# Optimization experiments

Hardware: AMD Instinct MI355X
Metric: run time of the kernel (lower is better)

## Reference

```python
import jax, jax.numpy as jnp
import numpy as np

B, T, EMB = 2, 2048, 1024
H, D = 16, 64          # n_heads, head_dim; H*D == EMB
FF = 4 * EMB


def _ln(x, w, b, eps=1e-5):
    mu = jnp.mean(x, axis=-1, keepdims=True)
    var = jnp.var(x, axis=-1, keepdims=True)
    return (x - mu) * jax.lax.rsqrt(var + eps) * w + b


def setup_inputs() -> dict:
    key = jax.random.key(0)
    ks = jax.random.split(key, 5)
    s = 0.02
    return {
        "x": jax.random.normal(ks[0], (B, T, EMB), jnp.float32),
        "ln1_w": jnp.ones((EMB,), jnp.float32),
        "ln1_b": jnp.zeros((EMB,), jnp.float32),
        "c_proj_w": jax.random.normal(ks[1], (3 * H * D, EMB), jnp.float32) * s,  # Linear(emb, 3HD, bias=False)
        "proj_w": jax.random.normal(ks[2], (EMB, H * D), jnp.float32) * s,
        "proj_b": jnp.zeros((EMB,), jnp.float32),
        "ln2_w": jnp.ones((EMB,), jnp.float32),
        "ln2_b": jnp.zeros((EMB,), jnp.float32),
        "ffn1_w": jax.random.normal(ks[3], (FF, EMB), jnp.float32) * s,
        "ffn1_b": jnp.zeros((FF,), jnp.float32),
        "ffn2_w": jax.random.normal(ks[4], (EMB, FF), jnp.float32) * s,
        "ffn2_b": jnp.zeros((EMB,), jnp.float32),
    }


def reference(x, ln1_w, ln1_b, c_proj_w, proj_w, proj_b, ln2_w, ln2_b,
              ffn1_w, ffn1_b, ffn2_w, ffn2_b):
    Bx, Tx, C = x.shape
    ln_x = _ln(x, ln1_w, ln1_b)
    c = ln_x @ c_proj_w.T                     # (B,T,3HD)
    c = c.reshape(Bx, Tx, H, 3 * D)
    k, q, v = jnp.split(c, 3, axis=-1)        # split order k,q,v as in source
    q = q.transpose(0, 2, 1, 3)               # (B,H,T,D)
    k = k.transpose(0, 2, 1, 3)
    v = v.transpose(0, 2, 1, 3)
    wei = jnp.einsum('bhqd,bhkd->bhqk', q, k) * (D ** -0.5)  # (B,H,T,T)
    mask = jnp.tril(jnp.ones((Tx, Tx), bool))
    wei = jnp.where(mask, wei, -jnp.inf)
    wei = jax.nn.softmax(wei, axis=-1)
    act = jnp.einsum('bhqk,bhkd->bhqd', wei, v)
    act = act.transpose(0, 2, 1, 3).reshape(Bx, Tx, H * D)
    act = act @ proj_w.T + proj_b
    act = x + act                              # residual 1
    h = _ln(act, ln2_w, ln2_b)
    h = jax.nn.relu(h @ ffn1_w.T + ffn1_b) @ ffn2_w.T + ffn2_b
    return x + h                               # NOTE: source adds x, not act
```

## Files before the change

kernel.cpp:

```cpp
#include <hip/hip_runtime.h>
#include <math.h>

typedef unsigned short u16;
typedef unsigned int u32;
typedef __attribute__((ext_vector_type(8))) __bf16 bf16x8;
typedef __attribute__((ext_vector_type(4))) float f32x4;
typedef __attribute__((ext_vector_type(16))) float f32x16;

#define DEVI __device__ __forceinline__

DEVI u16 f2bf(float f){
  u32 b = __builtin_bit_cast(u32, f);
  return (u16)((b + 0x7FFFu + ((b >> 16) & 1u)) >> 16);
}

DEVI u32 cvtpk(float a, float b){
  u32 r;
  asm("v_cvt_pk_bf16_f32 %0, %1, %2" : "=v"(r) : "v"(a), "v"(b));
  return r;
}

DEVI f32x4 mfma16(bf16x8 a, bf16x8 b, f32x4 c){
  return __builtin_amdgcn_mfma_f32_16x16x32_bf16(a, b, c, 0, 0, 0);
}
DEVI f32x16 mfma32(bf16x8 a, bf16x8 b, f32x16 c){
  return __builtin_amdgcn_mfma_f32_32x32x16_bf16(a, b, c, 0, 0, 0);
}

DEVI void gload16(const u16* g, u16* l){
  __builtin_amdgcn_global_load_lds(
      (const __attribute__((address_space(1))) u32*)g,
      (__attribute__((address_space(3))) u32*)l,
      16, 0, 0);
}

DEVI void phase_bar(){
  __builtin_amdgcn_sched_barrier(0);
  __builtin_amdgcn_s_barrier();
  __builtin_amdgcn_sched_barrier(0);
}

DEVI bf16x8 scale_bf16x8(bf16x8 v, float s){
  u32 w[4]; __builtin_memcpy(w, &v, 16);
  u32 o[4];
  #pragma unroll
  for (int i = 0; i < 4; ++i){
    float f0 = __builtin_bit_cast(float, (w[i] & 0xFFFFu) << 16) * s;
    float f1 = __builtin_bit_cast(float, w[i] & 0xFFFF0000u) * s;
    o[i] = (u32)f2bf(f0) | ((u32)f2bf(f1) << 16);
  }
  bf16x8 r; __builtin_memcpy(&r, o, 16);
  return r;
}

DEVI void cvt_body(const float* __restrict__ in, u16* __restrict__ out, int i){
  float4 v = reinterpret_cast<const float4*>(in)[i];
  u32 lo = (u32)f2bf(v.x) | ((u32)f2bf(v.y) << 16);
  u32 hi = (u32)f2bf(v.z) | ((u32)f2bf(v.w) << 16);
  reinterpret_cast<uint2*>(out)[i] = make_uint2(lo, hi);
}

DEVI void ln_body(const float* __restrict__ x, const float* __restrict__ w,
                  const float* __restrict__ b, u16* __restrict__ out,
                  int row, int tid, float* red){
  const float4 v = reinterpret_cast<const float4*>(x + (size_t)row * 1024)[tid];
  float s  = v.x + v.y + v.z + v.w;
  float ss = v.x*v.x + v.y*v.y + v.z*v.z + v.w*v.w;
  #pragma unroll
  for (int m = 1; m < 64; m <<= 1){
    s  += __shfl_xor(s,  m, 64);
    ss += __shfl_xor(ss, m, 64);
  }
  int wid = tid >> 6, lane = tid & 63;
  if (lane == 0){ red[wid] = s; red[4 + wid] = ss; }
  __syncthreads();
  s  = red[0] + red[1] + red[2] + red[3];
  ss = red[4] + red[5] + red[6] + red[7];
  float mu   = s * (1.0f/1024.0f);
  float var  = ss * (1.0f/1024.0f) - mu*mu;
  float rstd = rsqrtf(var + 1e-5f);
  const float4 wv = reinterpret_cast<const float4*>(w)[tid];
  const float4 bv = reinterpret_cast<const float4*>(b)[tid];
  u32 lo = (u32)f2bf((v.x-mu)*rstd*wv.x + bv.x) | ((u32)f2bf((v.y-mu)*rstd*wv.y + bv.y) << 16);
  u32 hi = (u32)f2bf((v.z-mu)*rstd*wv.z + bv.z) | ((u32)f2bf((v.w-mu)*rstd*wv.w + bv.w) << 16);
  reinterpret_cast<uint2*>(out + (size_t)row*1024)[tid] = make_uint2(lo, hi);
}

__global__ __launch_bounds__(256) void prep_kernel(const float* __restrict__ c_proj_w,
                                                   const float* __restrict__ proj_w,
                                                   const float* __restrict__ ffn1_w,
                                                   const float* __restrict__ ffn2_w,
                                                   const float* __restrict__ x,
                                                   const float* __restrict__ ln1_w,
                                                   const float* __restrict__ ln1_b,
                                                   u16* __restrict__ Wqkv,
                                                   u16* __restrict__ Wproj,
                                                   u16* __restrict__ Wff1,
                                                   u16* __restrict__ Wff2,
                                                   u16* __restrict__ LNb){
  __shared__ float red[8];
  const int bid = blockIdx.x;
  const int tid = threadIdx.x;
  if (bid < 3072){
    cvt_body(c_proj_w, Wqkv, bid*256 + tid);
  } else if (bid < 4096){
    cvt_body(proj_w, Wproj, (bid - 3072)*256 + tid);
  } else if (bid < 8192){
    cvt_body(ffn1_w, Wff1, (bid - 4096)*256 + tid);
  } else if (bid < 12288){
    cvt_body(ffn2_w, Wff2, (bid - 8192)*256 + tid);
  } else {
    ln_body(x, ln1_w, ln1_b, LNb, bid - 12288, tid, red);
  }
}

__global__ __launch_bounds__(256) void ln_kernel(const float* __restrict__ x,
                                                 const float* __restrict__ w,
                                                 const float* __restrict__ b,
                                                 u16* __restrict__ out){
  __shared__ float red[8];
  ln_body(x, w, b, out, blockIdx.x, threadIdx.x, red);
}

__global__ __launch_bounds__(256) void reduce4_kernel(const u16* __restrict__ P,
                                                      const float* __restrict__ x,
                                                      const float* __restrict__ bias,
                                                      float* __restrict__ out){
  const size_t i8 = ((size_t)blockIdx.x * 256 + threadIdx.x) * 8;
  const size_t PS = (size_t)4096 * 1024;
  const int col0 = (int)(i8 & 1023);
  float acc[8];
  #pragma unroll
  for (int j = 0; j < 8; ++j) acc[j] = bias[col0 + j];
  #pragma unroll
  for (int s = 0; s < 4; ++s){
    uint4 d = *reinterpret_cast<const uint4*>(P + s*PS + i8);
    u32 w[4] = {d.x, d.y, d.z, d.w};
    #pragma unroll
    for (int j = 0; j < 8; ++j){
      u32 bits = ((w[j>>1] >> (16*(j&1))) & 0xFFFFu) << 16;
      acc[j] += __builtin_bit_cast(float, bits);
    }
  }
  float4 xv0 = reinterpret_cast<const float4*>(x + i8)[0];
  float4 xv1 = reinterpret_cast<const float4*>(x + i8)[1];
  acc[0]+=xv0.x; acc[1]+=xv0.y; acc[2]+=xv0.z; acc[3]+=xv0.w;
  acc[4]+=xv1.x; acc[5]+=xv1.y; acc[6]+=xv1.z; acc[7]+=xv1.w;
  reinterpret_cast<float4*>(out + i8)[0] = make_float4(acc[0],acc[1],acc[2],acc[3]);
  reinterpret_cast<float4*>(out + i8)[1] = make_float4(acc[4],acc[5],acc[6],acc[7]);
}

template<bool HAS_BIAS, bool RELU, bool SPLIT>
__global__ __launch_bounds__(512, 2) void gemm256(const u16* __restrict__ A,
                                                  const u16* __restrict__ W,
                                                  const float* __restrict__ bias,
                                                  u16* __restrict__ outp,
                                                  int M, int N, int lda, int kLen){
  const int tid = threadIdx.x;
  const int wid = tid >> 6, lane = tid & 63;
  const int l16 = lane & 15, lhi = lane >> 4;
  const int wr = wid >> 2, wc = wid & 3;

  const int gx = gridDim.x, gy = gridDim.y;
  const int nwg = gx * gy * gridDim.z;
  const int bid = (blockIdx.z * gy + blockIdx.y) * gx + blockIdx.x;
  const int swz = (bid & 7) * (nwg >> 3) + (bid >> 3);
  const int col = swz % gx;
  const int rs  = swz / gx;
  const int row = rs % gy;
  const int ksp = rs / gy;
  const int brow = row * 256;
  const int bcol = col * 256;
  const size_t koff = (size_t)ksp * kLen;
  if (SPLIT) outp += (size_t)ksp * M * N;

  __shared__ u16 LDS[2][2][2][256*32];

  const int srow = tid >> 2;
  const int cg   = (tid & 3) ^ ((tid >> 3) & 3);
  const u16* gA = A + (size_t)(brow + srow) * lda + koff + cg*8;
  const u16* gW = W + (size_t)(bcol + srow) * lda + koff + cg*8;
  const size_t rK = (size_t)128 * lda;

#define STAGE(buf, mat, ks, t) do {                                   \
    const u16* _s = ((mat) ? gW : gA) + (t)*64 + (ks)*32;             \
    u16* _d = &LDS[buf][mat][ks][(wid*16)*32];                        \
    gload16(_s,      _d);                                             \
    gload16(_s + rK, _d + 128*32);                                    \
  } while(0)

  const int cswz = (lhi ^ ((l16 >> 1) & 3)) * 8;
  const int aoff = (wr*128 + l16)*32 + cswz;
  const int boff = (wc*64  + l16)*32 + cswz;
#define RDA(buf, ks, m) (*reinterpret_cast<const bf16x8*>(&LDS[buf][0][ks][aoff + (m)*512]))
#define RDB(buf, ks, n) (*reinterpret_cast<const bf16x8*>(&LDS[buf][1][ks][boff + (n)*512]))

  f32x4 acc[8][4] = {};
  bf16x8 a[8], b0, b1;

#define MFMA_PH(n0, n1) do {                                          \
    __builtin_amdgcn_s_setprio(1);                                    \
    _Pragma("unroll")                                                 \
    for (int m = 0; m < 8; ++m){                                      \
      acc[m][n0] = mfma16(a[m], b0, acc[m][n0]);                      \
      acc[m][n1] = mfma16(a[m], b1, acc[m][n1]);                      \
    }                                                                 \
    __builtin_amdgcn_s_setprio(0);                                    \
  } while(0)

  const int NITER = kLen >> 7;

  STAGE(0,0,0,0); STAGE(0,1,0,0); STAGE(0,0,1,0); STAGE(0,1,1,0);
  STAGE(1,0,0,1); STAGE(1,1,0,1);
  asm volatile("s_waitcnt vmcnt(4)" ::: "memory");
  phase_bar();

  for (int j = 0; j < NITER; ++j){
    const int t0 = 2*j, t1 = 2*j + 1;
    const bool more = (j + 1 < NITER);

    #pragma unroll
    for (int m = 0; m < 8; ++m) a[m] = RDA(0,0,m);
    b0 = RDB(0,0,0); b1 = RDB(0,0,1);
    STAGE(1,0,1,t1);
    phase_bar();
    MFMA_PH(0,1);
    phase_bar();
    b0 = RDB(0,0,2); b1 = RDB(0,0,3);
    STAGE(1,1,1,t1);
    phase_bar();
    MFMA_PH(2,3);
    phase_bar();
    #pragma unroll
    for (int m = 0; m < 8; ++m) a[m] = RDA(0,1,m);
    b0 = RDB(0,1,0); b1 = RDB(0,1,1);
    if (more) STAGE(0,0,0,t0+2);
    phase_bar();
    MFMA_PH(0,1);
    phase_bar();
    b0 = RDB(0,1,2); b1 = RDB(0,1,3);
    if (more){ STAGE(0,1,0,t0+2); asm volatile("s_waitcnt vmcnt(4)" ::: "memory"); }
    else     {                    asm volatile("s_waitcnt vmcnt(0)" ::: "memory"); }
    phase_bar();
    MFMA_PH(2,3);
    phase_bar();
    #pragma unroll
    for (int m = 0; m < 8; ++m) a[m] = RDA(1,0,m);
    b0 = RDB(1,0,0); b1 = RDB(1,0,1);
    if (more) STAGE(0,0,1,t0+2);
    phase_bar();
    MFMA_PH(0,1);
    phase_bar();
    b0 = RDB(1,0,2); b1 = RDB(1,0,3);
    if (more) STAGE(0,1,1,t0+2);
    phase_bar();
    MFMA_PH(2,3);
    phase_bar();
    #pragma unroll
    for (int m = 0; m < 8; ++m) a[m] = RDA(1,1,m);
    b0 = RDB(1,1,0); b1 = RDB(1,1,1);
    if (more) STAGE(1,0,0,t1+2);
    phase_bar();
    MFMA_PH(0,1);
    phase_bar();
    b0 = RDB(1,1,2); b1 = RDB(1,1,3);
    if (more){ STAGE(1,1,0,t1+2); asm volatile("s_waitcnt vmcnt(4)" ::: "memory"); }
    phase_bar();
    MFMA_PH(2,3);
    phase_bar();
  }
  __builtin_amdgcn_sched_barrier(0);

  const int row0 = brow + wr*128;
  const int col0 = bcol + wc*64;
  #pragma unroll
  for (int m = 0; m < 8; ++m){
    #pragma unroll
    for (int n = 0; n < 4; ++n){
      #pragma unroll
      for (int r = 0; r < 4; ++r){
        int row_ = row0 + m*16 + 4*lhi + r;
        int col_ = col0 + n*16 + l16;
        float v = acc[m][n][r];
        if constexpr (HAS_BIAS) v += bias[col_];
        if constexpr (RELU)     v = fmaxf(v, 0.0f);
        outp[(size_t)row_ * N + col_] = f2bf(v);
      }
    }
  }
#undef STAGE
#undef RDA
#undef RDB
#undef MFMA_PH
}

template<bool HAS_BIAS, bool HAS_RES, bool RELU, bool OUT_BF16>
__global__ __launch_bounds__(256) void gemm_bt(const u16* __restrict__ A,
                                               const u16* __restrict__ W,
                                               const float* __restrict__ bias,
                                               const float* __restrict__ res,
                                               void* __restrict__ outp,
                                               int M, int N, int K){
  const int tid = threadIdx.x;
  const int wid = tid >> 6, lane = tid & 63;
  const int l16 = lane & 15, lhi = lane >> 4;
  const int wr = wid >> 1, wc = wid & 1;

  const int gx = gridDim.x;
  const int nwg = gx * gridDim.y;
  const int bid = blockIdx.y * gx + blockIdx.x;
  const int swz = (bid & 7) * (nwg >> 3) + (bid >> 3);
  const int brow = (swz / gx) * 128;
  const int bcol = (swz % gx) * 128;

  __shared__ u16 As[2][128*32];
  __shared__ u16 Bs[2][128*32];

  const int srow = wid*32 + (lane >> 2);
  const int schk = lane & 3;
  const u16* gA0 = A + (size_t)(brow + srow)      * K + schk*8;
  const u16* gA1 = A + (size_t)(brow + srow + 16) * K + schk*8;
  const u16* gW0 = W + (size_t)(bcol + srow)      * K + schk*8;
  const u16* gW1 = W + (size_t)(bcol + srow + 16) * K + schk*8;
  const int ldsA0 = (wid*32)*32, ldsA1 = (wid*32 + 16)*32;

  f32x4 acc[4][4] = {};

  gload16(gA0, &As[0][ldsA0]);
  gload16(gA1, &As[0][ldsA1]);
  gload16(gW0, &Bs[0][ldsA0]);
  gload16(gW1, &Bs[0][ldsA1]);

  int cur = 0;
  for (int k0 = 0; k0 < K; k0 += 32){
    __syncthreads();
    if (k0 + 32 < K){
      gload16(gA0 + k0 + 32, &As[cur^1][ldsA0]);
      gload16(gA1 + k0 + 32, &As[cur^1][ldsA1]);
      gload16(gW0 + k0 + 32, &Bs[cur^1][ldsA0]);
      gload16(gW1 + k0 + 32, &Bs[cur^1][ldsA1]);
    }
    bf16x8 af[4], bfr[4];
    #pragma unroll
    for (int m = 0; m < 4; ++m)
      af[m]  = *reinterpret_cast<const bf16x8*>(&As[cur][(wr*64 + m*16 + l16)*32 + 8*lhi]);
    #pragma unroll
    for (int n = 0; n < 4; ++n)
      bfr[n] = *reinterpret_cast<const bf16x8*>(&Bs[cur][(wc*64 + n*16 + l16)*32 + 8*lhi]);
    #pragma unroll
    for (int m = 0; m < 4; ++m){
      #pragma unroll
      for (int n = 0; n < 4; ++n){
        acc[m][n] = mfma16(af[m], bfr[n], acc[m][n]);
      }
    }
    cur ^= 1;
  }

  const int row0 = brow + wr*64;
  const int col0 = bcol + wc*64;
  #pragma unroll
  for (int m = 0; m < 4; ++m){
    #pragma unroll
    for (int n = 0; n < 4; ++n){
      #pragma unroll
      for (int r = 0; r < 4; ++r){
        int row = row0 + m*16 + 4*lhi + r;
        int col = col0 + n*16 + l16;
        float v = acc[m][n][r];
        if constexpr (HAS_BIAS) v += bias[col];
        if constexpr (RELU)     v = fmaxf(v, 0.0f);
        if constexpr (HAS_RES)  v += res[(size_t)row * N + col];
        if constexpr (OUT_BF16) ((u16*)outp)[(size_t)row * N + col] = f2bf(v);
        else                    ((float*)outp)[(size_t)row * N + col] = v;
      }
    }
  }
}

__global__ __launch_bounds__(128) void attn_kernel(const u16* __restrict__ qkv,
                                                   u16* __restrict__ att){
  const int bh = blockIdx.x;
  const int g  = 31 - blockIdx.y;
  const int bb = bh >> 4, hh = bh & 15;
  const int tid = threadIdx.x;
  const int wid = tid >> 6, lane = tid & 63;
  const int l31 = lane & 31, h = lane >> 5;
  const u16* base = qkv + (size_t)bb * 2048 * 3072 + (size_t)hh * 192;

  __shared__ u16 Ks[64*72];
  __shared__ u16 Vt[64*80];

  const int sr = tid >> 1, sh2 = (tid & 1) * 32;
  const u16* kstage = base + (size_t)sr * 3072 + sh2;
  const int va = tid >> 2, vd = (tid & 3) * 16;
  const u16* vstage = base + (size_t)(2*va) * 3072 + 128 + vd;

  const int qrow0 = g*64 + wid*32;
  const int q = qrow0 + l31;

  const float QSCALE = 0.125f * 1.44269504f;
  bf16x8 qb[4];
  {
    const u16* qp = base + (size_t)q * 3072 + 64 + 8*h;
    #pragma unroll
    for (int s = 0; s < 4; ++s)
      qb[s] = scale_bf16x8(*reinterpret_cast<const bf16x8*>(qp + 16*s), QSCALE);
  }

  f32x16 o0 = (f32x16)0.0f, o1 = (f32x16)0.0f;
  float m = -INFINITY, l = 0.0f;

  const int nkt = g + 1;

  uint4 ka0, ka1, ka2, ka3, v00, v01, v10, v11;
  ka0 = *reinterpret_cast<const uint4*>(kstage);
  ka1 = *reinterpret_cast<const uint4*>(kstage + 8);
  ka2 = *reinterpret_cast<const uint4*>(kstage + 16);
  ka3 = *reinterpret_cast<const uint4*>(kstage + 24);
  v00 = *reinterpret_cast<const uint4*>(vstage);
  v01 = *reinterpret_cast<const uint4*>(vstage + 8);
  v10 = *reinterpret_cast<const uint4*>(vstage + 3072);
  v11 = *reinterpret_cast<const uint4*>(vstage + 3072 + 8);

  for (int kt = 0; kt < nkt; ++kt){
    __syncthreads();
    *reinterpret_cast<uint4*>(&Ks[sr*72 + sh2])      = ka0;
    *reinterpret_cast<uint4*>(&Ks[sr*72 + sh2 + 8])  = ka1;
    *reinterpret_cast<uint4*>(&Ks[sr*72 + sh2 + 16]) = ka2;
    *reinterpret_cast<uint4*>(&Ks[sr*72 + sh2 + 24]) = ka3;
    {
      u32 w00[4] = {v00.x, v00.y, v00.z, v00.w};
      u32 w01[4] = {v01.x, v01.y, v01.z, v01.w};
      u32 w10[4] = {v10.x, v10.y, v10.z, v10.w};
      u32 w11[4] = {v11.x, v11.y, v11.z, v11.w};
      #pragma unroll
      for (int j = 0; j < 16; ++j){
        u32 e0 = ((j < 8 ? w00[j>>1] : w01[(j-8)>>1]) >> (16*(j&1))) & 0xFFFFu;
        u32 e1 = ((j < 8 ? w10[j>>1] : w11[(j-8)>>1]) >> (16*(j&1))) & 0xFFFFu;
        int d = vd + j;
        *reinterpret_cast<u32*>(&Vt[d*80 + (((va>>2) ^ (d>>3)) << 3) + 2*(va&3)]) =
            e0 | (e1 << 16);
      }
    }
    __syncthreads();

    if (kt + 1 < nkt){
      const u16* kp = kstage + (size_t)(kt + 1) * 64 * 3072;
      const u16* vp = vstage + (size_t)(kt + 1) * 64 * 3072;
      ka0 = *reinterpret_cast<const uint4*>(kp);
      ka1 = *reinterpret_cast<const uint4*>(kp + 8);
      ka2 = *reinterpret_cast<const uint4*>(kp + 16);
      ka3 = *reinterpret_cast<const uint4*>(kp + 24);
      v00 = *reinterpret_cast<const uint4*>(vp);
      v01 = *reinterpret_cast<const uint4*>(vp + 8);
      v10 = *reinterpret_cast<const uint4*>(vp + 3072);
      v11 = *reinterpret_cast<const uint4*>(vp + 3072 + 8);
    }

    f32x16 s0 = (f32x16)0.0f, s1 = (f32x16)0.0f;
    __builtin_amdgcn_s_setprio(1);
    #pragma unroll
    for (int s = 0; s < 4; ++s){
      bf16x8 kf0 = *reinterpret_cast<const bf16x8*>(&Ks[l31*72      + 16*s + 8*h]);
      bf16x8 kf1 = *reinterpret_cast<const bf16x8*>(&Ks[(32+l31)*72 + 16*s + 8*h]);
      s0 = mfma32(kf0, qb[s], s0);
      s1 = mfma32(kf1, qb[s], s1);
    }
    __builtin_amdgcn_s_setprio(0);

    if (kt == nkt - 1){
      #pragma unroll
      for (int r = 0; r < 16; ++r){
        int krow = kt*64 + (r&3) + 8*(r>>2) + 4*h;
        if (krow > q)      s0[r] = -INFINITY;
        if (krow + 32 > q) s1[r] = -INFINITY;
      }
    }

    float mx = s0[0];
    #pragma unroll
    for (int r = 1; r < 16; ++r) mx = fmaxf(mx, s0[r]);
    #pragma unroll
    for (int r = 0; r < 16; ++r) mx = fmaxf(mx, s1[r]);
    mx = fmaxf(mx, __shfl_xor(mx, 32, 64));
    if (__any(mx > m)){
      float mnew = fmaxf(m, mx);
      float al = exp2f(m - mnew);
      m = mnew;
      l *= al;
      o0 *= al;
      o1 *= al;
    }
    float p0[16], p1[16];
    float su = 0.0f;
    #pragma unroll
    for (int r = 0; r < 16; ++r){ p0[r] = exp2f(s0[r] - m); su += p0[r]; }
    #pragma unroll
    for (int r = 0; r < 16; ++r){ p1[r] = exp2f(s1[r] - m); su += p1[r]; }
    l += su;

    u32 pk0[8], pk1[8];
    #pragma unroll
    for (int g4 = 0; g4 < 4; ++g4){
      pk0[2*g4]   = cvtpk(p0[4*g4],   p0[4*g4+1]);
      pk0[2*g4+1] = cvtpk(p0[4*g4+2], p0[4*g4+3]);
      pk1[2*g4]   = cvtpk(p1[4*g4],   p1[4*g4+1]);
      pk1[2*g4+1] = cvtpk(p1[4*g4+2], p1[4*g4+3]);
    }

    __builtin_amdgcn_s_setprio(1);
    #pragma unroll
    for (int s = 0; s < 4; ++s){
      const int gA = (s & 1) * 2;
      u32 oa0 = (s >> 1) ? pk1[2*gA]       : pk0[2*gA];
      u32 oa1 = (s >> 1) ? pk1[2*gA+1]     : pk0[2*gA+1];
      u32 ob0 = (s >> 1) ? pk1[2*(gA+1)]   : pk0[2*(gA+1)];
      u32 ob1 = (s >> 1) ? pk1[2*(gA+1)+1] : pk0[2*(gA+1)+1];
      u32 t0 = h ? oa0 : ob0;
      u32 t1 = h ? oa1 : ob1;
      u32 r0 = (u32)__shfl_xor((int)t0, 32, 64);
      u32 r1 = (u32)__shfl_xor((int)t1, 32, 64);
      u32 b0_ = h ? r0 : oa0;
      u32 b1_ = h ? r1 : oa1;
      u32 b2_ = h ? ob0 : r0;
      u32 b3_ = h ? ob1 : r1;
      bf16x8 pfrag = __builtin_bit_cast(bf16x8, make_uint4(b0_, b1_, b2_, b3_));
      bf16x8 vf0 = *reinterpret_cast<const bf16x8*>(
          &Vt[l31*80      + (((2*s + h) ^ (l31 >> 3)) << 3)]);
      bf16x8 vf1 = *reinterpret_cast<const bf16x8*>(
          &Vt[(32+l31)*80 + (((2*s + h) ^ ((32+l31) >> 3)) << 3)]);
      o0 = mfma32(vf0, pfrag, o0);
      o1 = mfma32(vf1, pfrag, o1);
    }
    __builtin_amdgcn_s_setprio(0);
  }

  l += __shfl_xor(l, 32, 64);
  float inv = 1.0f / l;
  u16* orow = att + (size_t)(bb*2048 + q) * 1024 + hh*64;
  #pragma unroll
  for (int r = 0; r < 16; r += 2){
    int d0 = (r&3) + 8*(r>>2) + 4*h;
    *reinterpret_cast<u32*>(&orow[d0])      = cvtpk(o0[r]*inv, o0[r+1]*inv);
    *reinterpret_cast<u32*>(&orow[32 + d0]) = cvtpk(o1[r]*inv, o1[r+1]*inv);
  }
}

extern "C" void kernel_launch(void* const* d_in, const int* in_sizes, int n_in,
                              void* d_out, int out_size, void* d_ws, size_t ws_size,
                              hipStream_t stream){
  const float* x        = (const float*)d_in[0];
  const float* ln1_w    = (const float*)d_in[1];
  const float* ln1_b    = (const float*)d_in[2];
  const float* c_proj_w = (const float*)d_in[3];
  const float* proj_w   = (const float*)d_in[4];
  const float* proj_b   = (const float*)d_in[5];
  const float* ln2_w    = (const float*)d_in[6];
  const float* ln2_b    = (const float*)d_in[7];
  const float* ffn1_w   = (const float*)d_in[8];
  const float* ffn1_b   = (const float*)d_in[9];
  const float* ffn2_w   = (const float*)d_in[10];
  const float* ffn2_b   = (const float*)d_in[11];

  char* p = (char*)d_ws;
  u16* Wff1  = (u16*)p;  p += (size_t)4096*1024*2;
  u16* Wff2  = (u16*)p;  p += (size_t)1024*4096*2;
  u16* QKV   = (u16*)p;  p += (size_t)4096*3072*2;
  u16* ATT   = (u16*)p;  p += (size_t)4096*1024*2;
  u16* Wqkv  = (u16*)p;  p += (size_t)3072*1024*2;
  u16* Wproj = (u16*)p;  p += (size_t)1024*1024*2;
  u16* LNb   = (u16*)p;  p += (size_t)4096*1024*2;
  float* ACT2= (float*)p;
  u16* FFN1  = QKV;
  u16* PART  = Wqkv;

  prep_kernel<<<16384, 256, 0, stream>>>(c_proj_w, proj_w, ffn1_w, ffn2_w,
                                         x, ln1_w, ln1_b,
                                         Wqkv, Wproj, Wff1, Wff2, LNb);
  gemm256<false,false,false><<<dim3(12,16,1), 512, 0, stream>>>(LNb, Wqkv, nullptr, QKV, 4096, 3072, 1024, 1024);
  attn_kernel<<<dim3(32,32), 128, 0, stream>>>(QKV, ATT);
  gemm_bt<true ,true ,false,false><<<dim3(8,32), 256, 0, stream>>>(ATT, Wproj, proj_b, x, ACT2, 4096, 1024, 1024);
  ln_kernel<<<4096, 256, 0, stream>>>(ACT2, ln2_w, ln2_b, LNb);
  gemm256<true ,true ,false><<<dim3(16,16,1), 512, 0, stream>>>(LNb, Wff1, ffn1_b, FFN1, 4096, 4096, 1024, 1024);
  gemm256<false,false,true ><<<dim3(4,16,4), 512, 0, stream>>>(FFN1, Wff2, nullptr, PART, 4096, 1024, 4096, 1024);
  reduce4_kernel<<<2048, 256, 0, stream>>>(PART, x, ffn2_b, (float*)d_out);
}
```

Measured before the change: 234.1 us.

## Double-buffer K/V shared-memory tiles in causal attention kernel

Makes the K and V^T shared-memory tiles double-buffered. Each iteration writes the next tile into the alternate buffer and issues global loads two tiles ahead, then computes on the current buffer. This cuts the per-iteration barriers from two to one and lets LDS writes overlap with MFMA work. In exchange it doubles LDS use, which may lower occupancy, and holds prefetched registers across a longer span.

```diff
diff --git a/kernel.cpp b/kernel.cpp
--- a/kernel.cpp
+++ b/kernel.cpp
@@ -388,8 +388,8 @@
   const int l31 = lane & 31, h = lane >> 5;
   const u16* base = qkv + (size_t)bb * 2048 * 3072 + (size_t)hh * 192;
 
-  __shared__ u16 Ks[64*72];
-  __shared__ u16 Vt[64*80];
+  __shared__ u16 Ks[2][64*72];
+  __shared__ u16 Vt[2][64*80];
 
   const int sr = tid >> 1, sh2 = (tid & 1) * 32;
   const u16* kstage = base + (size_t)sr * 3072 + sh2;
@@ -414,56 +414,60 @@
   const int nkt = g + 1;
 
   uint4 ka0, ka1, ka2, ka3, v00, v01, v10, v11;
-  ka0 = *reinterpret_cast<const uint4*>(kstage);
-  ka1 = *reinterpret_cast<const uint4*>(kstage + 8);
-  ka2 = *reinterpret_cast<const uint4*>(kstage + 16);
-  ka3 = *reinterpret_cast<const uint4*>(kstage + 24);
-  v00 = *reinterpret_cast<const uint4*>(vstage);
-  v01 = *reinterpret_cast<const uint4*>(vstage + 8);
-  v10 = *reinterpret_cast<const uint4*>(vstage + 3072);
-  v11 = *reinterpret_cast<const uint4*>(vstage + 3072 + 8);
+#define LOADREGS(t) do {                                               \
+    const u16* kp = kstage + (size_t)(t) * 64 * 3072;                  \
+    const u16* vp = vstage + (size_t)(t) * 64 * 3072;                  \
+    ka0 = *reinterpret_cast<const uint4*>(kp);                         \
+    ka1 = *reinterpret_cast<const uint4*>(kp + 8);                     \
+    ka2 = *reinterpret_cast<const uint4*>(kp + 16);                    \
+    ka3 = *reinterpret_cast<const uint4*>(kp + 24);                    \
+    v00 = *reinterpret_cast<const uint4*>(vp);                         \
+    v01 = *reinterpret_cast<const uint4*>(vp + 8);                     \
+    v10 = *reinterpret_cast<const uint4*>(vp + 3072);                  \
+    v11 = *reinterpret_cast<const uint4*>(vp + 3072 + 8);              \
+  } while(0)
+
+#define WRITE_TILE(B) do {                                             \
+    *reinterpret_cast<uint4*>(&Ks[B][sr*72 + sh2])      = ka0;         \
+    *reinterpret_cast<uint4*>(&Ks[B][sr*72 + sh2 + 8])  = ka1;         \
+    *reinterpret_cast<uint4*>(&Ks[B][sr*72 + sh2 + 16]) = ka2;         \
+    *reinterpret_cast<uint4*>(&Ks[B][sr*72 + sh2 + 24]) = ka3;         \
+    u32 w00[4] = {v00.x, v00.y, v00.z, v00.w};                         \
+    u32 w01[4] = {v01.x, v01.y, v01.z, v01.w};                         \
+    u32 w10[4] = {v10.x, v10.y, v10.z, v10.w};                         \
+    u32 w11[4] = {v11.x, v11.y, v11.z, v11.w};                         \
+    _Pragma("unroll")                                                  \
+    for (int j = 0; j < 16; ++j){                                      \
+      u32 e0 = ((j < 8 ? w00[j>>1] : w01[(j-8)>>1]) >> (16*(j&1))) & 0xFFFFu; \
+      u32 e1 = ((j < 8 ? w10[j>>1] : w11[(j-8)>>1]) >> (16*(j&1))) & 0xFFFFu; \
+      int d = vd + j;                                                  \
+      *reinterpret_cast<u32*>(&Vt[B][d*80 + (((va>>2) ^ (d>>3)) << 3) + 2*(va&3)]) = \
+          e0 | (e1 << 16);                                             \
+    }                                                                  \
+  } while(0)
+
+  LOADREGS(0);
+  WRITE_TILE(0);
+  __syncthreads();
+  if (nkt > 1) LOADREGS(1);
 
   for (int kt = 0; kt < nkt; ++kt){
-    __syncthreads();
-    *reinterpret_cast<uint4*>(&Ks[sr*72 + sh2])      = ka0;
-    *reinterpret_cast<uint4*>(&Ks[sr*72 + sh2 + 8])  = ka1;
-    *reinterpret_cast<uint4*>(&Ks[sr*72 + sh2 + 16]) = ka2;
-    *reinterpret_cast<uint4*>(&Ks[sr*72 + sh2 + 24]) = ka3;
-    {
-      u32 w00[4] = {v00.x, v00.y, v00.z, v00.w};
-      u32 w01[4] = {v01.x, v01.y, v01.z, v01.w};
-      u32 w10[4] = {v10.x, v10.y, v10.z, v10.w};
-      u32 w11[4] = {v11.x, v11.y, v11.z, v11.w};
-      #pragma unroll
-      for (int j = 0; j < 16; ++j){
-        u32 e0 = ((j < 8 ? w00[j>>1] : w01[(j-8)>>1]) >> (16*(j&1))) & 0xFFFFu;
-        u32 e1 = ((j < 8 ? w10[j>>1] : w11[(j-8)>>1]) >> (16*(j&1))) & 0xFFFFu;
-        int d = vd + j;
-        *reinterpret_cast<u32*>(&Vt[d*80 + (((va>>2) ^ (d>>3)) << 3) + 2*(va&3)]) =
-            e0 | (e1 << 16);
-      }
-    }
-    __syncthreads();
+    const int cur = kt & 1;
 
     if (kt + 1 < nkt){
-      const u16* kp = kstage + (size_t)(kt + 1) * 64 * 3072;
-      const u16* vp = vstage + (size_t)(kt + 1) * 64 * 3072;
-      ka0 = *reinterpret_cast<const uint4*>(kp);
-      ka1 = *reinterpret_cast<const uint4*>(kp + 8);
-      ka2 = *reinterpret_cast<const uint4*>(kp + 16);
-      ka3 = *reinterpret_cast<const uint4*>(kp + 24);
-      v00 = *reinterpret_cast<const uint4*>(vp);
-      v01 = *reinterpret_cast<const uint4*>(vp + 8);
-      v10 = *reinterpret_cast<const uint4*>(vp + 3072);
-      v11 = *reinterpret_cast<const uint4*>(vp + 3072 + 8);
-    }
+      WRITE_TILE(cur ^ 1);
+      if (kt + 2 < nkt) LOADREGS(kt + 2);
+    }
+
+    const u16* KsC = &Ks[cur][0];
+    const u16* VtC = &Vt[cur][0];
 
     f32x16 s0 = (f32x16)0.0f, s1 = (f32x16)0.0f;
     __builtin_amdgcn_s_setprio(1);
     #pragma unroll
     for (int s = 0; s < 4; ++s){
-      bf16x8 kf0 = *reinterpret_cast<const bf16x8*>(&Ks[l31*72      + 16*s + 8*h]);
-      bf16x8 kf1 = *reinterpret_cast<const bf16x8*>(&Ks[(32+l31)*72 + 16*s + 8*h]);
+      bf16x8 kf0 = *reinterpret_cast<const bf16x8*>(&KsC[l31*72      + 16*s + 8*h]);
+      bf16x8 kf1 = *reinterpret_cast<const bf16x8*>(&KsC[(32+l31)*72 + 16*s + 8*h]);
       s0 = mfma32(kf0, qb[s], s0);
       s1 = mfma32(kf1, qb[s], s1);
     }
@@ -527,13 +531,15 @@
       u32 b3_ = h ? ob1 : r1;
       bf16x8 pfrag = __builtin_bit_cast(bf16x8, make_uint4(b0_, b1_, b2_, b3_));
       bf16x8 vf0 = *reinterpret_cast<const bf16x8*>(
-          &Vt[l31*80      + (((2*s + h) ^ (l31 >> 3)) << 3)]);
+          &VtC[l31*80      + (((2*s + h) ^ (l31 >> 3)) << 3)]);
       bf16x8 vf1 = *reinterpret_cast<const bf16x8*>(
-          &Vt[(32+l31)*80 + (((2*s + h) ^ ((32+l31) >> 3)) << 3)]);
+          &VtC[(32+l31)*80 + (((2*s + h) ^ ((32+l31) >> 3)) << 3)]);
       o0 = mfma32(vf0, pfrag, o0);
       o1 = mfma32(vf1, pfrag, o1);
     }
     __builtin_amdgcn_s_setprio(0);
+
+    __syncthreads();
   }
 
   l += __shfl_xor(l, 32, 64);
@@ -545,6 +551,8 @@
     *reinterpret_cast<u32*>(&orow[d0])      = cvtpk(o0[r]*inv, o0[r+1]*inv);
     *reinterpret_cast<u32*>(&orow[32 + d0]) = cvtpk(o1[r]*inv, o1[r+1]*inv);
   }
+#undef LOADREGS
+#undef WRITE_TILE
 }
 
 extern "C" void kernel_launch(void* const* d_in, const int* in_sizes, int n_in,
```

New measurement: 235.7 us. About the same (+0.7%).
